# Optimization experiments

Measured on AMD Instinct MI355X. Metric: run time of the kernel, lower is better.

The kernel has to match this reference:

```python
import jax, jax.numpy as jnp
import numpy as np

DIM = 2048
H = 16          # n_heads
HKV = 4         # n_kv_heads
NREP = H // HKV
ROPE_D = 64
NOPE_D = 128
V_D = 128
QK_D = ROPE_D + NOPE_D
KV_RANK = 512
Q_RANK = 1536
B, T = 2, 2048


def _rope_cache(seq_len, head_dim, dtype=jnp.float32):
    # theta over even dims, angles concatenated [ang, ang] -> [T, head_dim]
    theta = 1.0 / (10000.0 ** (jnp.arange(0, head_dim, 2, dtype=dtype) / head_dim))
    pos = jnp.arange(seq_len, dtype=dtype)
    ang = jnp.outer(pos, theta)
    ang = jnp.concatenate([ang, ang], axis=-1)
    return jnp.cos(ang), jnp.sin(ang)  # each [T, head_dim]


def _rotate_half(x):
    half = x.shape[-1] // 2
    return jnp.concatenate([-x[..., half:], x[..., :half]], axis=-1)


def _apply_rope(x, cos, sin):
    # x: [B, T, h, d]; cos/sin: [T, d] broadcast over batch and heads
    return x * cos[None, :, None, :] + _rotate_half(x) * sin[None, :, None, :]


def setup_inputs() -> dict:
    key = jax.random.key(0)
    ks = jax.random.split(key, 9)
    s = 0.02
    return {
        "x": jax.random.normal(ks[0], (B, T, DIM), jnp.float32),
        "W_kv_down": jax.random.normal(ks[1], (DIM, KV_RANK), jnp.float32) * s,
        "W_k_nope": jax.random.normal(ks[2], (KV_RANK, HKV * NOPE_D), jnp.float32) * s,
        "W_k_rope": jax.random.normal(ks[3], (KV_RANK, HKV * ROPE_D), jnp.float32) * s,
        "W_v": jax.random.normal(ks[4], (KV_RANK, HKV * V_D), jnp.float32) * s,
        "W_q_down": jax.random.normal(ks[5], (DIM, Q_RANK), jnp.float32) * s,
        "W_q_nope": jax.random.normal(ks[6], (Q_RANK, H * NOPE_D), jnp.float32) * s,
        "W_q_rope": jax.random.normal(ks[7], (Q_RANK, H * ROPE_D), jnp.float32) * s,
        "W_o": jax.random.normal(ks[8], (H * V_D, DIM), jnp.float32) * s,
    }


def reference(x, W_kv_down, W_k_nope, W_k_rope, W_v, W_q_down, W_q_nope, W_q_rope, W_o):
    Bx, Tx, _ = x.shape
    scale = 1.0 / np.sqrt(QK_D)

    kv_c = x @ W_kv_down                                        # [B,T,KV_RANK]
    k_nope = (kv_c @ W_k_nope).reshape(Bx, Tx, HKV, NOPE_D)
    k_rope = (kv_c @ W_k_rope).reshape(Bx, Tx, HKV, ROPE_D)
    v = (kv_c @ W_v).reshape(Bx, Tx, HKV, V_D)

    q_c = x @ W_q_down                                          # [B,T,Q_RANK]
    q_nope = (q_c @ W_q_nope).reshape(Bx, Tx, H, NOPE_D)
    q_rope = (q_c @ W_q_rope).reshape(Bx, Tx, H, ROPE_D)

    cos, sin = _rope_cache(Tx, ROPE_D, x.dtype)
    q_rope = _apply_rope(q_rope, cos, sin)
    k_rope = _apply_rope(k_rope, cos, sin)

    q = jnp.concatenate([q_nope, q_rope], axis=-1).transpose(0, 2, 1, 3)  # [B,H,T,QK_D]
    k = jnp.concatenate([k_nope, k_rope], axis=-1).transpose(0, 2, 1, 3)  # [B,HKV,T,QK_D]
    vh = v.transpose(0, 2, 1, 3)                                          # [B,HKV,T,V_D]

    k = jnp.repeat(k, NREP, axis=1)   # GQA repeat -> [B,H,T,QK_D]
    vh = jnp.repeat(vh, NREP, axis=1)

    attn = jnp.einsum("bhqd,bhkd->bhqk", q, k) * scale
    causal = jnp.triu(jnp.ones((Tx, Tx), dtype=bool), k=1)
    attn = jnp.where(causal[None, None], -jnp.inf, attn)
    attn = jax.nn.softmax(attn, axis=-1)

    out = jnp.einsum("bhqk,bhkd->bhqd", attn, vh)               # [B,H,T,V_D]
    out = out.transpose(0, 2, 1, 3).reshape(Bx, Tx, H * V_D)
    return out @ W_o
```

## Files before the change

### kernel.cpp

```cpp
#include <hip/hip_runtime.h>
#include <hip/hip_bf16.h>

typedef __bf16 bf16;
typedef __attribute__((ext_vector_type(8))) __bf16 bf16x8;
typedef __attribute__((ext_vector_type(4))) __bf16 bf16x4;
typedef __attribute__((ext_vector_type(4))) float f32x4;

#define NH 16
#define NKV 4
#define ROPE_DIM 64
#define NOPE_DIM 128
#define V_DIM 128
#define QK_DIM 192
#define TT 2048
#define BB 2
#define MM 4096

#define QK_SCALE 0.07216878364870323f

__device__ __forceinline__ void gload16(const bf16* g, bf16* l) {
    __builtin_amdgcn_global_load_lds(
        (const __attribute__((address_space(1))) void*)g,
        (__attribute__((address_space(3))) void*)l, 16, 0, 0);
}

__global__ __launch_bounds__(256) void k_cvt(const float* __restrict__ s,
                                             bf16* __restrict__ d, int n4) {
    int idx = blockIdx.x * 256 + threadIdx.x;
    int stride = gridDim.x * 256;
    for (int i = idx; i < n4; i += stride) {
        float4 v = *(const float4*)(s + (size_t)i * 4);
        bf16* o = d + (size_t)i * 4;
        o[0] = (bf16)v.x; o[1] = (bf16)v.y; o[2] = (bf16)v.z; o[3] = (bf16)v.w;
    }
}

__global__ __launch_bounds__(256) void k_trc(const float* __restrict__ s,
                                             bf16* __restrict__ d, int R, int C) {
    __shared__ float tile[32][33];
    int tx = threadIdx.x & 31, ty = threadIdx.x >> 5;
    int c0 = blockIdx.x * 32, r0 = blockIdx.y * 32;
    #pragma unroll
    for (int rr = ty; rr < 32; rr += 8)
        tile[rr][tx] = s[(size_t)(r0 + rr) * C + c0 + tx];
    __syncthreads();
    #pragma unroll
    for (int cc = ty; cc < 32; cc += 8)
        d[(size_t)(c0 + cc) * R + r0 + tx] = (bf16)tile[tx][cc];
}

__global__ __launch_bounds__(256) void k_rope_tab(float* __restrict__ ct,
                                                  float* __restrict__ st) {
    int idx = blockIdx.x * 256 + threadIdx.x;
    if (idx >= TT * 32) return;
    int t = idx >> 5, i = idx & 31;
    float theta = powf(10000.f, -(float)(2 * i) / 64.f);
    float ang = (float)t * theta;
    ct[idx] = cosf(ang);
    st[idx] = sinf(ang);
}

template<bool F32OUT>
__global__ __launch_bounds__(256) void k_gemm(const bf16* __restrict__ A, int lda,
                                              const bf16* __restrict__ Bt, int ldb,
                                              void* __restrict__ Cv, int ldc,
                                              int M, int N, int K) {
    __shared__ __align__(16) bf16 As[128 * 32];
    __shared__ __align__(16) bf16 Bs[128 * 32];
    const int tid = threadIdx.x;
    const int lane = tid & 63;
    const int wid = tid >> 6;
    const int wr = wid >> 1, wc = wid & 1;
    const int g = lane >> 4, c = lane & 15;
    const int m0 = blockIdx.y * 128, n0 = blockIdx.x * 128;

    f32x4 acc[4][4] = {};
    const int rdswz = (g ^ ((c >> 1) & 3)) * 8;

    for (int k0 = 0; k0 < K; k0 += 32) {
        __syncthreads();
        #pragma unroll
        for (int i = 0; i < 2; i++) {
            int ch = tid + 256 * i;
            int row = ch >> 2;
            int kc = (ch & 3) ^ ((ch >> 3) & 3);
            gload16(A + (size_t)(m0 + row) * lda + k0 + kc * 8, &As[ch * 8]);
            gload16(Bt + (size_t)(n0 + row) * ldb + k0 + kc * 8, &Bs[ch * 8]);
        }
        __syncthreads();
        bf16x8 af[4], bfr[4];
        #pragma unroll
        for (int i = 0; i < 4; i++)
            af[i] = *(const bf16x8*)&As[(wr * 64 + i * 16 + c) * 32 + rdswz];
        #pragma unroll
        for (int j = 0; j < 4; j++)
            bfr[j] = *(const bf16x8*)&Bs[(wc * 64 + j * 16 + c) * 32 + rdswz];
        #pragma unroll
        for (int i = 0; i < 4; i++)
            #pragma unroll
            for (int j = 0; j < 4; j++)
                acc[i][j] = __builtin_amdgcn_mfma_f32_16x16x32_bf16(
                    af[i], bfr[j], acc[i][j], 0, 0, 0);
    }

    #pragma unroll
    for (int i = 0; i < 4; i++) {
        int row = m0 + wr * 64 + i * 16 + g * 4;
        #pragma unroll
        for (int j = 0; j < 4; j++) {
            int col = n0 + wc * 64 + j * 16 + c;
            #pragma unroll
            for (int r = 0; r < 4; r++) {
                if (F32OUT)
                    ((float*)Cv)[(size_t)(row + r) * ldc + col] = acc[i][j][r];
                else
                    ((bf16*)Cv)[(size_t)(row + r) * ldc + col] = (bf16)acc[i][j][r];
            }
        }
    }
}

__global__ __launch_bounds__(256) void k_asm_q(const bf16* __restrict__ C3,
                                               const float* __restrict__ ct,
                                               const float* __restrict__ st,
                                               bf16* __restrict__ qa) {
    int row = blockIdx.x;
    int b = row >> 11, t = row & 2047;
    for (int e = threadIdx.x; e < NH * QK_DIM; e += 256) {
        int h = e / QK_DIM, d = e % QK_DIM;
        bf16 val;
        if (d < NOPE_DIM) {
            val = (bf16)((float)C3[(size_t)row * 3072 + h * NOPE_DIM + d] * QK_SCALE);
        } else {
            int dr = d - NOPE_DIM, i = dr & 31;
            float cs = ct[t * 32 + i], sn = st[t * 32 + i];
            const bf16* base = C3 + (size_t)row * 3072 + 2048 + h * ROPE_DIM;
            float xv = (float)base[dr];
            float ov = (dr < 32) ? -(float)base[dr + 32] : (float)base[dr - 32];
            val = (bf16)((xv * cs + ov * sn) * QK_SCALE);
        }
        qa[((size_t)(b * NH + h) * TT + t) * QK_DIM + d] = val;
    }
}

__global__ __launch_bounds__(256) void k_asm_k(const bf16* __restrict__ C2,
                                               const float* __restrict__ ct,
                                               const float* __restrict__ st,
                                               bf16* __restrict__ ka) {
    int row = blockIdx.x;
    int b = row >> 11, t = row & 2047;
    for (int e = threadIdx.x; e < NKV * QK_DIM; e += 256) {
        int h = e / QK_DIM, d = e % QK_DIM;
        bf16 val;
        if (d < NOPE_DIM) {
            val = C2[(size_t)row * 1280 + h * NOPE_DIM + d];
        } else {
            int dr = d - NOPE_DIM, i = dr & 31;
            float cs = ct[t * 32 + i], sn = st[t * 32 + i];
            const bf16* base = C2 + (size_t)row * 1280 + 512 + h * ROPE_DIM;
            float xv = (float)base[dr];
            float ov = (dr < 32) ? -(float)base[dr + 32] : (float)base[dr - 32];
            val = (bf16)(xv * cs + ov * sn);
        }
        ka[((size_t)(b * NKV + h) * TT + t) * QK_DIM + d] = val;
    }
}

__global__ __launch_bounds__(256) void k_tr_v(const bf16* __restrict__ C2,
                                              bf16* __restrict__ vt) {
    __shared__ bf16 tile[32][33];
    int tx = threadIdx.x & 31, ty = threadIdx.x >> 5;
    int t0 = blockIdx.x * 32;
    int d0 = (blockIdx.y & 3) * 32;
    int bh = blockIdx.y >> 2;
    int b = bh >> 2, hk = bh & 3;
    const bf16* src = C2 + ((size_t)(b * TT + t0)) * 1280 + 768 + hk * V_DIM + d0;
    #pragma unroll
    for (int rr = ty; rr < 32; rr += 8)
        tile[rr][tx] = src[(size_t)rr * 1280 + tx];
    __syncthreads();
    bf16* dst = vt + ((size_t)bh * V_DIM + d0) * TT + t0;
    #pragma unroll
    for (int cc = ty; cc < 32; cc += 8)
        dst[(size_t)cc * TT + tx] = tile[tx][cc];
}

__global__ __launch_bounds__(256, 2) void k_attn(const bf16* __restrict__ qa,
                                                 const bf16* __restrict__ ka,
                                                 const bf16* __restrict__ vt,
                                                 bf16* __restrict__ out) {
    __shared__ __align__(16) bf16 Klds[64 * QK_DIM];
    __shared__ __align__(16) bf16 Vlds[128 * 64];
    __shared__ __align__(16) bf16 Plds[4][32 * 64];

    const int tid  = threadIdx.x;
    const int lane = tid & 63;
    const int wid  = tid >> 6;
    const int g = lane >> 4, c = lane & 15;
    const int hsw = c & 7;

    const int qi = (blockIdx.y & 16) ? (15 - (int)blockIdx.x) : (int)blockIdx.x;
    const int q0 = qi * 128;
    const int bh = blockIdx.y;
    const int b = bh >> 4, h = bh & 15;
    const int kv = b * NKV + (h >> 2);
    const int qb0 = q0 + wid * 32;

    bf16x8 qf[2][6];
    #pragma unroll
    for (int qs = 0; qs < 2; ++qs) {
        const bf16* qp = qa + ((size_t)bh * TT + qb0 + qs * 16 + c) * QK_DIM + g * 8;
        #pragma unroll
        for (int cc = 0; cc < 6; ++cc) qf[qs][cc] = *(const bf16x8*)(qp + cc * 32);
    }

    f32x4 accO[2][8] = {};
    float m[2] = {-1e30f, -1e30f};
    float l[2] = {0.f, 0.f};

    const bf16* kbase = ka + (size_t)kv * TT * QK_DIM;
    const bf16* vbase = vt + (size_t)kv * V_DIM * TT;

    const int nk = 2 * qi + 2;
    for (int it = 0; it < nk; ++it) {
        const int k0 = it * 64;
        __syncthreads();
        #pragma unroll
        for (int i = 0; i < 6; ++i) {
            int ch = tid + 256 * i;
            int row = ch / 24, cs = ch % 24;
            int gc = cs ^ (row & 7);
            gload16(kbase + (size_t)(k0 + row) * QK_DIM + gc * 8, &Klds[ch * 8]);
        }
        #pragma unroll
        for (int i = 0; i < 4; ++i) {
            int ch = tid + 256 * i;
            int row = ch >> 3, cs = ch & 7;
            int gc = cs ^ (row & 7);
            gload16(vbase + (size_t)row * TT + k0 + gc * 8, &Vlds[ch * 8]);
        }
        __syncthreads();

        if (k0 > qb0 + 15) continue;
        const bool a1 = (k0 <= qb0 + 31);

        f32x4 s[2][4] = {};
        #pragma unroll
        for (int cc = 0; cc < 6; ++cc) {
            #pragma unroll
            for (int j = 0; j < 4; ++j) {
                bf16x8 kf = *(const bf16x8*)&Klds[(j * 16 + c) * QK_DIM +
                                                  ((4 * cc + g) ^ hsw) * 8];
                s[0][j] = __builtin_amdgcn_mfma_f32_16x16x32_bf16(kf, qf[0][cc], s[0][j], 0, 0, 0);
                s[1][j] = __builtin_amdgcn_mfma_f32_16x16x32_bf16(kf, qf[1][cc], s[1][j], 0, 0, 0);
            }
        }

        #pragma unroll
        for (int qs = 0; qs < 2; ++qs) {
            if (qs == 1 && !a1) break;
            const int qb = qb0 + qs * 16;
            if (k0 + 63 > qb) {
                #pragma unroll
                for (int j = 0; j < 4; ++j)
                    #pragma unroll
                    for (int r = 0; r < 4; ++r)
                        if (k0 + j * 16 + g * 4 + r > qb + c) s[qs][j][r] = -1e30f;
            }
            float pmax = -1e30f;
            #pragma unroll
            for (int j = 0; j < 4; ++j)
                #pragma unroll
                for (int r = 0; r < 4; ++r) pmax = fmaxf(pmax, s[qs][j][r]);
            pmax = fmaxf(pmax, __shfl_xor(pmax, 16, 64));
            pmax = fmaxf(pmax, __shfl_xor(pmax, 32, 64));

            if (!__all(pmax <= m[qs] + 8.f)) {
                float mn = fmaxf(m[qs], pmax);
                float al = __expf(m[qs] - mn);
                m[qs] = mn;
                l[qs] *= al;
                #pragma unroll
                for (int nj = 0; nj < 8; ++nj)
                    #pragma unroll
                    for (int r = 0; r < 4; ++r) accO[qs][nj][r] *= al;
            }
            float ps = 0.f;
            #pragma unroll
            for (int j = 0; j < 4; ++j) {
                bf16x4 pk;
                #pragma unroll
                for (int r = 0; r < 4; ++r) {
                    float e = __expf(s[qs][j][r] - m[qs]);
                    ps += e;
                    pk[r] = (bf16)e;
                }
                *(bf16x4*)&Plds[wid][(qs * 16 + c) * 64 +
                                     ((j * 16 + g * 4) ^ (hsw * 8))] = pk;
            }
            ps += __shfl_xor(ps, 16, 64);
            ps += __shfl_xor(ps, 32, 64);
            l[qs] += ps;
        }

        if (a1) {
            #pragma unroll
            for (int kc = 0; kc < 2; ++kc) {
                bf16x8 pf0 = *(const bf16x8*)&Plds[wid][(c)      * 64 + ((kc * 32 + g * 8) ^ (hsw * 8))];
                bf16x8 pf1 = *(const bf16x8*)&Plds[wid][(16 + c) * 64 + ((kc * 32 + g * 8) ^ (hsw * 8))];
                #pragma unroll
                for (int nj = 0; nj < 8; ++nj) {
                    bf16x8 vf = *(const bf16x8*)&Vlds[(nj * 16 + c) * 64 +
                                                      ((4 * kc + g) ^ hsw) * 8];
                    accO[0][nj] = __builtin_amdgcn_mfma_f32_16x16x32_bf16(vf, pf0, accO[0][nj], 0, 0, 0);
                    accO[1][nj] = __builtin_amdgcn_mfma_f32_16x16x32_bf16(vf, pf1, accO[1][nj], 0, 0, 0);
                }
            }
        } else {
            #pragma unroll
            for (int kc = 0; kc < 2; ++kc) {
                bf16x8 pf0 = *(const bf16x8*)&Plds[wid][(c) * 64 + ((kc * 32 + g * 8) ^ (hsw * 8))];
                #pragma unroll
                for (int nj = 0; nj < 8; ++nj) {
                    bf16x8 vf = *(const bf16x8*)&Vlds[(nj * 16 + c) * 64 +
                                                      ((4 * kc + g) ^ hsw) * 8];
                    accO[0][nj] = __builtin_amdgcn_mfma_f32_16x16x32_bf16(vf, pf0, accO[0][nj], 0, 0, 0);
                }
            }
        }
    }

    #pragma unroll
    for (int qs = 0; qs < 2; ++qs) {
        float inv = 1.f / l[qs];
        size_t rowoff = ((size_t)(b * TT + qb0 + qs * 16 + c)) * (NH * V_DIM) + h * V_DIM;
        #pragma unroll
        for (int nj = 0; nj < 8; ++nj) {
            bf16x4 o;
            #pragma unroll
            for (int r = 0; r < 4; ++r) o[r] = (bf16)(accO[qs][nj][r] * inv);
            *(bf16x4*)&out[rowoff + nj * 16 + g * 4] = o;
        }
    }
}

extern "C" void kernel_launch(void* const* d_in, const int* in_sizes, int n_in,
                              void* d_out, int out_size, void* d_ws, size_t ws_size,
                              hipStream_t stream) {
    const float* x    = (const float*)d_in[0];
    const float* Wkvd = (const float*)d_in[1];
    const float* Wkn  = (const float*)d_in[2];
    const float* Wkr  = (const float*)d_in[3];
    const float* Wv   = (const float*)d_in[4];
    const float* Wqd  = (const float*)d_in[5];
    const float* Wqn  = (const float*)d_in[6];
    const float* Wqr  = (const float*)d_in[7];
    const float* Wo   = (const float*)d_in[8];

    char* p = (char*)d_ws;
    size_t off = 0;
    auto take = [&](size_t elems, size_t esz) -> void* {
        void* r = p + off;
        off += ((elems * esz + 255) / 256) * 256;
        return r;
    };

    bf16* XB  = (bf16*)take((size_t)MM * 2048, 2);
    bf16* BT1 = (bf16*)take((size_t)2048 * 2048, 2);
    bf16* BT2 = (bf16*)take((size_t)1280 * 512, 2);
    bf16* BT3 = (bf16*)take((size_t)3072 * 1536, 2);
    bf16* BTO = (bf16*)take((size_t)2048 * 2048, 2);
    bf16* C1  = (bf16*)take((size_t)MM * 2048, 2);
    bf16* C2  = (bf16*)take((size_t)MM * 1280, 2);
    bf16* C3  = (bf16*)take((size_t)MM * 3072, 2);
    bf16* QA  = (bf16*)take((size_t)BB * NH * TT * QK_DIM, 2);
    bf16* KA  = (bf16*)take((size_t)BB * NKV * TT * QK_DIM, 2);
    bf16* VT  = (bf16*)take((size_t)BB * NKV * V_DIM * TT, 2);
    bf16* AO  = (bf16*)take((size_t)MM * 2048, 2);
    float* CT = (float*)take((size_t)TT * 32, 4);
    float* ST = (float*)take((size_t)TT * 32, 4);
    (void)ws_size; (void)in_sizes; (void)n_in; (void)out_size;

    k_cvt<<<2048, 256, 0, stream>>>(x, XB, MM * 2048 / 4);
    k_trc<<<dim3(512 / 32, 2048 / 32), 256, 0, stream>>>(Wkvd, BT1, 2048, 512);
    k_trc<<<dim3(1536 / 32, 2048 / 32), 256, 0, stream>>>(Wqd, BT1 + (size_t)512 * 2048, 2048, 1536);
    k_trc<<<dim3(512 / 32, 512 / 32), 256, 0, stream>>>(Wkn, BT2, 512, 512);
    k_trc<<<dim3(256 / 32, 512 / 32), 256, 0, stream>>>(Wkr, BT2 + (size_t)512 * 512, 512, 256);
    k_trc<<<dim3(512 / 32, 512 / 32), 256, 0, stream>>>(Wv, BT2 + (size_t)768 * 512, 512, 512);
    k_trc<<<dim3(2048 / 32, 1536 / 32), 256, 0, stream>>>(Wqn, BT3, 1536, 2048);
    k_trc<<<dim3(1024 / 32, 1536 / 32), 256, 0, stream>>>(Wqr, BT3 + (size_t)2048 * 1536, 1536, 1024);
    k_trc<<<dim3(2048 / 32, 2048 / 32), 256, 0, stream>>>(Wo, BTO, 2048, 2048);
    k_rope_tab<<<(TT * 32) / 256, 256, 0, stream>>>(CT, ST);

    k_gemm<false><<<dim3(2048 / 128, MM / 128), 256, 0, stream>>>(XB, 2048, BT1, 2048, C1, 2048, MM, 2048, 2048);
    k_gemm<false><<<dim3(1280 / 128, MM / 128), 256, 0, stream>>>(C1, 2048, BT2, 512, C2, 1280, MM, 1280, 512);
    k_gemm<false><<<dim3(3072 / 128, MM / 128), 256, 0, stream>>>(C1 + 512, 2048, BT3, 1536, C3, 3072, MM, 3072, 1536);

    k_asm_q<<<MM, 256, 0, stream>>>(C3, CT, ST, QA);
    k_asm_k<<<MM, 256, 0, stream>>>(C2, CT, ST, KA);
    k_tr_v<<<dim3(TT / 32, 4 * BB * NKV), 256, 0, stream>>>(C2, VT);

    k_attn<<<dim3(16, BB * NH), 256, 0, stream>>>(QA, KA, VT, AO);

    k_gemm<true><<<dim3(2048 / 128, MM / 128), 256, 0, stream>>>(AO, 2048, BTO, 2048, d_out, 2048, MM, 2048, 2048);
}
```

Before: 455.0 us.

## Fuse weight prep into one kernel and QKV assembly into GEMM epilogues

Merges all weight transposes, the RoPE table and the input conversion into a single prep kernel dispatched by block index. The K/V and Q projection GEMMs now apply RoPE, scaling and head-major layout (and the V transpose) directly in their epilogues, so the C2/C3 intermediates and three assembly kernels are removed. This cuts launch count and an intermediate write/read round trip. The cost is more complex epilogues with strided scattered stores and extra table loads inside the GEMM.

Measured after the change: 412.2 us. -9.4%, faster.

```diff
diff --git a/kernel.cpp b/kernel.cpp
--- a/kernel.cpp
+++ b/kernel.cpp
@@ -24,47 +24,64 @@
         (__attribute__((address_space(3))) void*)l, 16, 0, 0);
 }
 
-__global__ __launch_bounds__(256) void k_cvt(const float* __restrict__ s,
-                                             bf16* __restrict__ d, int n4) {
-    int idx = blockIdx.x * 256 + threadIdx.x;
-    int stride = gridDim.x * 256;
-    for (int i = idx; i < n4; i += stride) {
-        float4 v = *(const float4*)(s + (size_t)i * 4);
-        bf16* o = d + (size_t)i * 4;
+struct PrepArgs {
+    const float* wsrc[8];
+    bf16* wdst[8];
+    const float* x;
+    bf16* xb;
+    float* ct;
+    float* st;
+};
+
+__global__ __launch_bounds__(256) void k_prep(PrepArgs a) {
+    constexpr int WR[8] = {2048, 2048, 512, 512, 512, 1536, 1536, 2048};
+    constexpr int WC[8] = {512, 1536, 512, 256, 512, 2048, 1024, 2048};
+    const int bid = blockIdx.x;
+    if (bid < 13440) {
+        int w = 0, base = 0;
+        #pragma unroll
+        for (int i = 0; i < 8; i++) {
+            int t = (WC[i] >> 5) * (WR[i] >> 5);
+            if (w == i && bid >= base + t) { base += t; w = i + 1; }
+        }
+        const int local = bid - base;
+        const int R = WR[w], C = WC[w];
+        const int tilesX = C >> 5;
+        const int tyt = local / tilesX, txt = local - tyt * tilesX;
+        const int c0 = txt * 32, r0 = tyt * 32;
+        const float* s = a.wsrc[w];
+        bf16* d = a.wdst[w];
+        __shared__ float tile[32][33];
+        int tx = threadIdx.x & 31, ty = threadIdx.x >> 5;
+        #pragma unroll
+        for (int rr = ty; rr < 32; rr += 8)
+            tile[rr][tx] = s[(size_t)(r0 + rr) * C + c0 + tx];
+        __syncthreads();
+        #pragma unroll
+        for (int cc = ty; cc < 32; cc += 8)
+            d[(size_t)(c0 + cc) * R + r0 + tx] = (bf16)tile[tx][cc];
+    } else if (bid < 13696) {
+        int idx = (bid - 13440) * 256 + threadIdx.x;
+        int t = idx >> 5, i = idx & 31;
+        float theta = powf(10000.f, -(float)(2 * i) / 64.f);
+        float ang = (float)t * theta;
+        a.ct[idx] = cosf(ang);
+        a.st[idx] = sinf(ang);
+    } else {
+        int i = (bid - 13696) * 256 + threadIdx.x;
+        float4 v = *(const float4*)(a.x + (size_t)i * 4);
+        bf16* o = a.xb + (size_t)i * 4;
         o[0] = (bf16)v.x; o[1] = (bf16)v.y; o[2] = (bf16)v.z; o[3] = (bf16)v.w;
     }
 }
 
-__global__ __launch_bounds__(256) void k_trc(const float* __restrict__ s,
-                                             bf16* __restrict__ d, int R, int C) {
-    __shared__ float tile[32][33];
-    int tx = threadIdx.x & 31, ty = threadIdx.x >> 5;
-    int c0 = blockIdx.x * 32, r0 = blockIdx.y * 32;
-    #pragma unroll
-    for (int rr = ty; rr < 32; rr += 8)
-        tile[rr][tx] = s[(size_t)(r0 + rr) * C + c0 + tx];
-    __syncthreads();
-    #pragma unroll
-    for (int cc = ty; cc < 32; cc += 8)
-        d[(size_t)(c0 + cc) * R + r0 + tx] = (bf16)tile[tx][cc];
-}
-
-__global__ __launch_bounds__(256) void k_rope_tab(float* __restrict__ ct,
-                                                  float* __restrict__ st) {
-    int idx = blockIdx.x * 256 + threadIdx.x;
-    if (idx >= TT * 32) return;
-    int t = idx >> 5, i = idx & 31;
-    float theta = powf(10000.f, -(float)(2 * i) / 64.f);
-    float ang = (float)t * theta;
-    ct[idx] = cosf(ang);
-    st[idx] = sinf(ang);
-}
-
-template<bool F32OUT>
+template<int EPI>
 __global__ __launch_bounds__(256) void k_gemm(const bf16* __restrict__ A, int lda,
                                               const bf16* __restrict__ Bt, int ldb,
-                                              void* __restrict__ Cv, int ldc,
-                                              int M, int N, int K) {
+                                              void* __restrict__ Cv, int ldc, int K,
+                                              const float* __restrict__ ct,
+                                              const float* __restrict__ st,
+                                              bf16* __restrict__ vt) {
     __shared__ __align__(16) bf16 As[128 * 32];
     __shared__ __align__(16) bf16 Bs[128 * 32];
     const int tid = threadIdx.x;
@@ -103,86 +120,86 @@
                     af[i], bfr[j], acc[i][j], 0, 0, 0);
     }
 
-    #pragma unroll
-    for (int i = 0; i < 4; i++) {
-        int row = m0 + wr * 64 + i * 16 + g * 4;
-        #pragma unroll
-        for (int j = 0; j < 4; j++) {
-            int col = n0 + wc * 64 + j * 16 + c;
-            #pragma unroll
-            for (int r = 0; r < 4; r++) {
-                if (F32OUT)
-                    ((float*)Cv)[(size_t)(row + r) * ldc + col] = acc[i][j][r];
-                else
-                    ((bf16*)Cv)[(size_t)(row + r) * ldc + col] = (bf16)acc[i][j][r];
-            }
-        }
-    }
-}
-
-__global__ __launch_bounds__(256) void k_asm_q(const bf16* __restrict__ C3,
-                                               const float* __restrict__ ct,
-                                               const float* __restrict__ st,
-                                               bf16* __restrict__ qa) {
-    int row = blockIdx.x;
-    int b = row >> 11, t = row & 2047;
-    for (int e = threadIdx.x; e < NH * QK_DIM; e += 256) {
-        int h = e / QK_DIM, d = e % QK_DIM;
-        bf16 val;
-        if (d < NOPE_DIM) {
-            val = (bf16)((float)C3[(size_t)row * 3072 + h * NOPE_DIM + d] * QK_SCALE);
-        } else {
-            int dr = d - NOPE_DIM, i = dr & 31;
-            float cs = ct[t * 32 + i], sn = st[t * 32 + i];
-            const bf16* base = C3 + (size_t)row * 3072 + 2048 + h * ROPE_DIM;
-            float xv = (float)base[dr];
-            float ov = (dr < 32) ? -(float)base[dr + 32] : (float)base[dr - 32];
-            val = (bf16)((xv * cs + ov * sn) * QK_SCALE);
-        }
-        qa[((size_t)(b * NH + h) * TT + t) * QK_DIM + d] = val;
-    }
-}
-
-__global__ __launch_bounds__(256) void k_asm_k(const bf16* __restrict__ C2,
-                                               const float* __restrict__ ct,
-                                               const float* __restrict__ st,
-                                               bf16* __restrict__ ka) {
-    int row = blockIdx.x;
-    int b = row >> 11, t = row & 2047;
-    for (int e = threadIdx.x; e < NKV * QK_DIM; e += 256) {
-        int h = e / QK_DIM, d = e % QK_DIM;
-        bf16 val;
-        if (d < NOPE_DIM) {
-            val = C2[(size_t)row * 1280 + h * NOPE_DIM + d];
-        } else {
-            int dr = d - NOPE_DIM, i = dr & 31;
-            float cs = ct[t * 32 + i], sn = st[t * 32 + i];
-            const bf16* base = C2 + (size_t)row * 1280 + 512 + h * ROPE_DIM;
-            float xv = (float)base[dr];
-            float ov = (dr < 32) ? -(float)base[dr + 32] : (float)base[dr - 32];
-            val = (bf16)(xv * cs + ov * sn);
-        }
-        ka[((size_t)(b * NKV + h) * TT + t) * QK_DIM + d] = val;
-    }
-}
-
-__global__ __launch_bounds__(256) void k_tr_v(const bf16* __restrict__ C2,
-                                              bf16* __restrict__ vt) {
-    __shared__ bf16 tile[32][33];
-    int tx = threadIdx.x & 31, ty = threadIdx.x >> 5;
-    int t0 = blockIdx.x * 32;
-    int d0 = (blockIdx.y & 3) * 32;
-    int bh = blockIdx.y >> 2;
-    int b = bh >> 2, hk = bh & 3;
-    const bf16* src = C2 + ((size_t)(b * TT + t0)) * 1280 + 768 + hk * V_DIM + d0;
-    #pragma unroll
-    for (int rr = ty; rr < 32; rr += 8)
-        tile[rr][tx] = src[(size_t)rr * 1280 + tx];
-    __syncthreads();
-    bf16* dst = vt + ((size_t)bh * V_DIM + d0) * TT + t0;
-    #pragma unroll
-    for (int cc = ty; cc < 32; cc += 8)
-        dst[(size_t)cc * TT + tx] = tile[tx][cc];
+    if constexpr (EPI <= 1) {
+        #pragma unroll
+        for (int i = 0; i < 4; i++) {
+            int row = m0 + wr * 64 + i * 16 + g * 4;
+            #pragma unroll
+            for (int j = 0; j < 4; j++) {
+                int col = n0 + wc * 64 + j * 16 + c;
+                #pragma unroll
+                for (int r = 0; r < 4; r++) {
+                    if (EPI == 1)
+                        ((float*)Cv)[(size_t)(row + r) * ldc + col] = acc[i][j][r];
+                    else
+                        ((bf16*)Cv)[(size_t)(row + r) * ldc + col] = (bf16)acc[i][j][r];
+                }
+            }
+        }
+    } else if constexpr (EPI == 2) {
+        bf16* ka = (bf16*)Cv;
+        #pragma unroll
+        for (int i = 0; i < 4; i++) {
+            int row = m0 + wr * 64 + i * 16 + g * 4;
+            int bq = row >> 11, t0 = row & 2047;
+            #pragma unroll
+            for (int j = 0; j < 4; j++) {
+                int col = n0 + wc * 64 + j * 16 + c;
+                if (col < 512) {
+                    int h = col >> 7, d = col & 127;
+                    bf16* dst = ka + ((size_t)(bq * NKV + h) * TT + t0) * QK_DIM + d;
+                    #pragma unroll
+                    for (int r = 0; r < 4; r++) dst[r * QK_DIM] = (bf16)acc[i][j][r];
+                } else if (col < 768) {
+                    int cr = col - 512;
+                    int h = cr >> 6, dr = cr & 63, ia = dr & 31;
+                    float sgn = (dr < 32) ? -1.f : 1.f;
+                    bf16* dst = ka + ((size_t)(bq * NKV + h) * TT + t0) * QK_DIM + 128 + dr;
+                    #pragma unroll
+                    for (int r = 0; r < 4; r++) {
+                        float cs = ct[(t0 + r) * 32 + ia], sn = st[(t0 + r) * 32 + ia];
+                        dst[r * QK_DIM] = (bf16)(acc[i][j][r] * cs + sgn * acc[i][j ^ 2][r] * sn);
+                    }
+                } else {
+                    int cr = col - 768;
+                    int h = cr >> 7, d = cr & 127;
+                    bf16x4 pk;
+                    #pragma unroll
+                    for (int r = 0; r < 4; r++) pk[r] = (bf16)acc[i][j][r];
+                    *(bf16x4*)&vt[((size_t)((bq * NKV + h) * V_DIM + d)) * TT + t0] = pk;
+                }
+            }
+        }
+    } else {
+        bf16* qa = (bf16*)Cv;
+        #pragma unroll
+        for (int i = 0; i < 4; i++) {
+            int row = m0 + wr * 64 + i * 16 + g * 4;
+            int bq = row >> 11, t0 = row & 2047;
+            #pragma unroll
+            for (int j = 0; j < 4; j++) {
+                int col = n0 + wc * 64 + j * 16 + c;
+                if (col < 2048) {
+                    int h = col >> 7, d = col & 127;
+                    bf16* dst = qa + ((size_t)(bq * NH + h) * TT + t0) * QK_DIM + d;
+                    #pragma unroll
+                    for (int r = 0; r < 4; r++)
+                        dst[r * QK_DIM] = (bf16)(acc[i][j][r] * QK_SCALE);
+                } else {
+                    int cr = col - 2048;
+                    int h = cr >> 6, dr = cr & 63, ia = dr & 31;
+                    float sgn = (dr < 32) ? -1.f : 1.f;
+                    bf16* dst = qa + ((size_t)(bq * NH + h) * TT + t0) * QK_DIM + 128 + dr;
+                    #pragma unroll
+                    for (int r = 0; r < 4; r++) {
+                        float cs = ct[(t0 + r) * 32 + ia], sn = st[(t0 + r) * 32 + ia];
+                        dst[r * QK_DIM] =
+                            (bf16)((acc[i][j][r] * cs + sgn * acc[i][j ^ 2][r] * sn) * QK_SCALE);
+                    }
+                }
+            }
+        }
+    }
 }
 
 __global__ __launch_bounds__(256, 2) void k_attn(const bf16* __restrict__ qa,
@@ -348,14 +365,6 @@
                               void* d_out, int out_size, void* d_ws, size_t ws_size,
                               hipStream_t stream) {
     const float* x    = (const float*)d_in[0];
-    const float* Wkvd = (const float*)d_in[1];
-    const float* Wkn  = (const float*)d_in[2];
-    const float* Wkr  = (const float*)d_in[3];
-    const float* Wv   = (const float*)d_in[4];
-    const float* Wqd  = (const float*)d_in[5];
-    const float* Wqn  = (const float*)d_in[6];
-    const float* Wqr  = (const float*)d_in[7];
-    const float* Wo   = (const float*)d_in[8];
 
     char* p = (char*)d_ws;
     size_t off = 0;
@@ -371,8 +380,6 @@
     bf16* BT3 = (bf16*)take((size_t)3072 * 1536, 2);
     bf16* BTO = (bf16*)take((size_t)2048 * 2048, 2);
     bf16* C1  = (bf16*)take((size_t)MM * 2048, 2);
-    bf16* C2  = (bf16*)take((size_t)MM * 1280, 2);
-    bf16* C3  = (bf16*)take((size_t)MM * 3072, 2);
     bf16* QA  = (bf16*)take((size_t)BB * NH * TT * QK_DIM, 2);
     bf16* KA  = (bf16*)take((size_t)BB * NKV * TT * QK_DIM, 2);
     bf16* VT  = (bf16*)take((size_t)BB * NKV * V_DIM * TT, 2);
@@ -381,26 +388,27 @@
     float* ST = (float*)take((size_t)TT * 32, 4);
     (void)ws_size; (void)in_sizes; (void)n_in; (void)out_size;
 
-    k_cvt<<<2048, 256, 0, stream>>>(x, XB, MM * 2048 / 4);
-    k_trc<<<dim3(512 / 32, 2048 / 32), 256, 0, stream>>>(Wkvd, BT1, 2048, 512);
-    k_trc<<<dim3(1536 / 32, 2048 / 32), 256, 0, stream>>>(Wqd, BT1 + (size_t)512 * 2048, 2048, 1536);
-    k_trc<<<dim3(512 / 32, 512 / 32), 256, 0, stream>>>(Wkn, BT2, 512, 512);
-    k_trc<<<dim3(256 / 32, 512 / 32), 256, 0, stream>>>(Wkr, BT2 + (size_t)512 * 512, 512, 256);
-    k_trc<<<dim3(512 / 32, 512 / 32), 256, 0, stream>>>(Wv, BT2 + (size_t)768 * 512, 512, 512);
-    k_trc<<<dim3(2048 / 32, 1536 / 32), 256, 0, stream>>>(Wqn, BT3, 1536, 2048);
-    k_trc<<<dim3(1024 / 32, 1536 / 32), 256, 0, stream>>>(Wqr, BT3 + (size_t)2048 * 1536, 1536, 1024);
-    k_trc<<<dim3(2048 / 32, 2048 / 32), 256, 0, stream>>>(Wo, BTO, 2048, 2048);
-    k_rope_tab<<<(TT * 32) / 256, 256, 0, stream>>>(CT, ST);
-
-    k_gemm<false><<<dim3(2048 / 128, MM / 128), 256, 0, stream>>>(XB, 2048, BT1, 2048, C1, 2048, MM, 2048, 2048);
-    k_gemm<false><<<dim3(1280 / 128, MM / 128), 256, 0, stream>>>(C1, 2048, BT2, 512, C2, 1280, MM, 1280, 512);
-    k_gemm<false><<<dim3(3072 / 128, MM / 128), 256, 0, stream>>>(C1 + 512, 2048, BT3, 1536, C3, 3072, MM, 3072, 1536);
-
-    k_asm_q<<<MM, 256, 0, stream>>>(C3, CT, ST, QA);
-    k_asm_k<<<MM, 256, 0, stream>>>(C2, CT, ST, KA);
-    k_tr_v<<<dim3(TT / 32, 4 * BB * NKV), 256, 0, stream>>>(C2, VT);
+    PrepArgs pa;
+    pa.wsrc[0] = (const float*)d_in[1]; pa.wdst[0] = BT1;
+    pa.wsrc[1] = (const float*)d_in[5]; pa.wdst[1] = BT1 + (size_t)512 * 2048;
+    pa.wsrc[2] = (const float*)d_in[2]; pa.wdst[2] = BT2;
+    pa.wsrc[3] = (const float*)d_in[3]; pa.wdst[3] = BT2 + (size_t)512 * 512;
+    pa.wsrc[4] = (const float*)d_in[4]; pa.wdst[4] = BT2 + (size_t)768 * 512;
+    pa.wsrc[5] = (const float*)d_in[6]; pa.wdst[5] = BT3;
+    pa.wsrc[6] = (const float*)d_in[7]; pa.wdst[6] = BT3 + (size_t)2048 * 1536;
+    pa.wsrc[7] = (const float*)d_in[8]; pa.wdst[7] = BTO;
+    pa.x = x; pa.xb = XB; pa.ct = CT; pa.st = ST;
+    k_prep<<<21888, 256, 0, stream>>>(pa);
+
+    k_gemm<0><<<dim3(16, 32), 256, 0, stream>>>(XB, 2048, BT1, 2048, C1, 2048, 2048,
+                                                nullptr, nullptr, nullptr);
+    k_gemm<2><<<dim3(10, 32), 256, 0, stream>>>(C1, 2048, BT2, 512, KA, 0, 512,
+                                                CT, ST, VT);
+    k_gemm<3><<<dim3(24, 32), 256, 0, stream>>>(C1 + 512, 2048, BT3, 1536, QA, 0, 1536,
+                                                CT, ST, nullptr);
 
     k_attn<<<dim3(16, BB * NH), 256, 0, stream>>>(QA, KA, VT, AO);
 
-    k_gemm<true><<<dim3(2048 / 128, MM / 128), 256, 0, stream>>>(AO, 2048, BTO, 2048, d_out, 2048, MM, 2048, 2048);
+    k_gemm<1><<<dim3(16, 32), 256, 0, stream>>>(AO, 2048, BTO, 2048, d_out, 2048, 2048,
+                                                nullptr, nullptr, nullptr);
 }
```
